# Kernel optimization log

Measured on AMD Instinct MI355X. Metric: run time of the kernel, lower is better.

The kernel has to match this reference:

```python
import jax, jax.numpy as jnp
import numpy as np
from jax import lax

NX, NV = 16384, 512
DV = 8.0 / NV
NUEE_COEFF = 2.221e-7        # 4*pi/3 * c_kpre * logLambda_ee (n0=1e20/cc, logLambda_ee=10)
SC_MAX_STEPS, SC_RTOL, SC_ATOL = 3, 1e-8, 1e-12
TWO_PI = 2.0 * np.pi
FOUR_PI = 4.0 * np.pi


def setup_inputs() -> dict:
    key = jax.random.key(0)
    v = (jnp.arange(NV, dtype=jnp.float32) + 0.5) * DV            # cell-centered positive-v grid
    f0x = jax.random.uniform(key, (NX, NV), dtype=jnp.float32) + 0.1
    f0x = f0x * jnp.exp(-0.5 * v[None, :] ** 2)                   # positive, Maxwellian-ish
    return {"nu": jnp.asarray(1.0, jnp.float32),
            "f0x": f0x,
            "dt": jnp.asarray(1.0e6, jnp.float32),
            "v": v}


def _self_consistent_beta(f0x, v):
    """Fixed-point solve for beta so the discrete Maxwellian exp(-beta v^2/2)
    matches the discrete temperature <v^2>/3 of f0.  Vectorized over nx."""
    v2 = v * v
    v4 = v2 * v2
    T_f = jnp.sum(f0x * v4, -1) / (3.0 * jnp.sum(f0x * v2, -1))   # (nx,)
    beta0 = 1.0 / T_f

    def step(beta, _):
        fM = jnp.exp(-0.5 * beta[:, None] * v2[None, :])
        T_M = jnp.sum(fM * v4, -1) / (3.0 * jnp.sum(fM * v2, -1))
        beta_new = beta * T_M / T_f
        done = jnp.abs(beta_new - beta) <= SC_ATOL + SC_RTOL * jnp.abs(beta)
        return jnp.where(done, beta, beta_new), None

    beta, _ = lax.scan(step, beta0, None, length=SC_MAX_STEPS)
    return beta


def _fast_vfp_D(f0x, beta, v):
    """Rank-1 Bell-Sherlock kernel: D(eps) = sqrt(eps)*2*pi*sum(sqrt(eps') f dEps'),
    normalized by beta * (4*pi int v^2 f dv).  O(nv), not O(nv^2)."""
    v_edge = 0.5 * (v[1:] + v[:-1])
    eps_edge = 0.5 * v_edge ** 2
    sqrt_eps = jnp.sqrt(eps_edge)
    d_eps = v_edge * DV                                           # dEps = v dv
    f_edge = 0.5 * (f0x[:, 1:] + f0x[:, :-1])
    inner = TWO_PI * jnp.sum(sqrt_eps * f_edge * d_eps, -1, keepdims=True)
    n4pi = FOUR_PI * jnp.sum(f0x * (v * v), -1, keepdims=True) * DV
    return sqrt_eps * inner / (beta[:, None] * n4pi)              # (nx, nv-1)


def _thomas(a, b, c, d):
    """Batched tridiagonal Thomas solve. a,b,c,d: (nx,nv); a[:,0]=c[:,-1]=0."""
    aT, bT, cT, dT = a.T, b.T, c.T, d.T                           # (nv, nx)
    z = jnp.zeros((d.shape[0],), d.dtype)

    def fwd(carry, row):
        cp, dp = carry
        ai, bi, ci, di = row
        denom = bi - ai * cp
        cpn = ci / denom
        dpn = (di - ai * dp) / denom
        return (cpn, dpn), (cpn, dpn)

    _, (cps, dps) = lax.scan(fwd, (z, z), (aT, bT, cT, dT))

    def back(x_next, cd):
        cp, dp = cd
        x = dp - cp * x_next
        return x, x

    _, xs = lax.scan(back, z, (cps, dps), reverse=True)
    return xs.T


def _solve(nu, f0x, dt, v):
    v2 = v * v
    v_edge = 0.5 * (v[1:] + v[:-1])
    beta = _self_consistent_beta(f0x, v)
    D = _fast_vfp_D(f0x, beta, v)                                 # (nx, nv-1)
    C = v_edge[None, :]                                           # drift coeff at interior edges
    # Chang-Cooper: delta = 1/w - 1/(e^w - 1), w = C dv / D  (delta->0.5 as w->0)
    w = C * DV / D
    small = jnp.abs(w) < 1e-6
    ws = jnp.where(small, 1.0, w)
    delta = jnp.where(small, 0.5, 1.0 / ws - 1.0 / jnp.expm1(ws))
    lo = C * delta - D / DV                                       # flux coeff of f_j
    hi = C * (1.0 - delta) + D / DV                               # flux coeff of f_{j+1}
    w2 = v_edge ** 2                                              # spherical metric at edges
    w2lo, w2hi = w2 * lo, w2 * hi
    inv = 1.0 / (v2 * DV)
    zcol = jnp.zeros((f0x.shape[0], 1), f0x.dtype)
    # L f[j] = (w2_j F_j - w2_{j-1} F_{j-1}) / (v_j^2 dv), zero-flux at both ends
    diagL = (jnp.concatenate([w2lo, zcol], -1) - jnp.concatenate([zcol, w2hi], -1)) * inv
    subL = jnp.concatenate([zcol, -w2lo], -1) * inv
    supL = jnp.concatenate([w2hi, zcol], -1) * inv
    k = dt * NUEE_COEFF                                           # implicit Euler: (I - dt*nu_ee*L) f = f0
    return _thomas(-k * subL, 1.0 - k * diagL, -k * supL, f0x)


def reference(nu, f0x, dt, v):
    return _solve(nu, f0x, dt, v)
```

## Files before the change

kernel.cpp:

```cpp
#include <hip/hip_runtime.h>

#define NVP 512

constexpr float DV_F   = 0.015625f;
constexpr float NUEE   = 2.221e-07f;
constexpr float TWOPI  = 6.283185307179586f;
constexpr float FOURPI = 12.566370614359172f;
constexpr float SQ05   = 0.7071067811865476f;

__device__ __forceinline__ float bf2f(unsigned int b) {
  return __uint_as_float(b << 16);
}

__global__ __launch_bounds__(256, 2)
void vfp_solve(const void* __restrict__ f0x_raw,
               const void* __restrict__ dt_raw,
               const void* __restrict__ v_raw,
               float* __restrict__ out,
               int nx)
{
  const int lane = threadIdx.x & 63;
  const int row  = (blockIdx.x << 2) + (threadIdx.x >> 6);
  if (row >= nx) return;

  const int j0 = lane * 8;

  const bool f32mode = (*(const unsigned int*)v_raw) == 0x3C000000u;

  float f[8], v[8];
  if (f32mode) {
    const float* fr = (const float*)f0x_raw + (size_t)row * NVP + j0;
    const float* vr = (const float*)v_raw + j0;
    float4 a0 = ((const float4*)fr)[0], a1 = ((const float4*)fr)[1];
    float4 b0 = ((const float4*)vr)[0], b1 = ((const float4*)vr)[1];
    f[0]=a0.x; f[1]=a0.y; f[2]=a0.z; f[3]=a0.w;
    f[4]=a1.x; f[5]=a1.y; f[6]=a1.z; f[7]=a1.w;
    v[0]=b0.x; v[1]=b0.y; v[2]=b0.z; v[3]=b0.w;
    v[4]=b1.x; v[5]=b1.y; v[6]=b1.z; v[7]=b1.w;
  } else {
    const unsigned short* fr = (const unsigned short*)f0x_raw + (size_t)row * NVP + j0;
    const unsigned short* vr = (const unsigned short*)v_raw + j0;
    uint4 fa = *(const uint4*)fr;
    uint4 va = *(const uint4*)vr;
    unsigned int w0[4] = {fa.x, fa.y, fa.z, fa.w};
    unsigned int w1[4] = {va.x, va.y, va.z, va.w};
#pragma unroll
    for (int q = 0; q < 4; ++q) {
      f[2*q]   = bf2f(w0[q] & 0xFFFFu);
      f[2*q+1] = bf2f(w0[q] >> 16);
      v[2*q]   = bf2f(w1[q] & 0xFFFFu);
      v[2*q+1] = bf2f(w1[q] >> 16);
    }
  }

  float dt;
  {
    float dA = f32mode ? *(const float*)dt_raw
                       : bf2f((unsigned int)(*(const unsigned short*)dt_raw));
    float dB = f32mode ? bf2f((unsigned int)(*(const unsigned short*)dt_raw))
                       : *(const float*)dt_raw;
    dt = (dA > 1.0e3f && dA < 1.0e9f) ? dA : dB;
  }
  const float kdt = dt * NUEE;

  float vprev = __shfl_up(v[7], 1);
  float vnext = __shfl_down(v[0], 1);

  float ve[9];
  ve[0] = 0.5f * (vprev + v[0]);
#pragma unroll
  for (int i = 1; i <= 7; ++i) ve[i] = 0.5f * (v[i-1] + v[i]);
  ve[8] = 0.5f * (v[7] + vnext);

  float v2[8];
#pragma unroll
  for (int i = 0; i < 8; ++i) v2[i] = v[i] * v[i];

  float s2 = 0.f, s4 = 0.f, sI = 0.f;
#pragma unroll
  for (int i = 0; i < 8; ++i) {
    int j = j0 + i;
    float fv2 = f[i] * v2[i];
    s2 += fv2;
    s4 += fv2 * v2[i];
    float ql = (j > 0)       ? SQ05 * ve[i]   * ve[i]   * DV_F : 0.f;
    float qr = (j < NVP - 1) ? SQ05 * ve[i+1] * ve[i+1] * DV_F : 0.f;
    sI += 0.5f * f[i] * (ql + qr);
  }
#pragma unroll
  for (int m = 32; m >= 1; m >>= 1) {
    s2 += __shfl_xor(s2, m);
    s4 += __shfl_xor(s4, m);
    sI += __shfl_xor(sI, m);
  }

  const float T_f = s4 / (3.0f * s2);
  float beta = 1.0f / T_f;

#pragma unroll
  for (int it = 0; it < 3; ++it) {
    float t2 = 0.f, t4 = 0.f;
#pragma unroll
    for (int i = 0; i < 8; ++i) {
      float fM = __expf(-0.5f * beta * v2[i]);
      float m2 = fM * v2[i];
      t2 += m2;
      t4 += m2 * v2[i];
    }
#pragma unroll
    for (int m = 32; m >= 1; m >>= 1) {
      t2 += __shfl_xor(t2, m);
      t4 += __shfl_xor(t4, m);
    }
    float T_M = t4 / (3.0f * t2);
    float bn = beta * (T_M / T_f);
    bool done = fabsf(bn - beta) <= 1e-12f + 1e-8f * fabsf(beta);
    beta = done ? beta : bn;
  }

  const float inner = TWOPI * sI;
  const float n4pi  = FOURPI * s2 * DV_F;
  const float Dfac  = inner / (beta * n4pi);
  const float X     = SQ05 * Dfac / DV_F;
  const float wv    = DV_F / (SQ05 * Dfac);
  float delta;
  if (fabsf(wv) < 1e-6f) delta = 0.5f;
  else                   delta = 1.0f / wv - 1.0f / expm1f(wv);
  const float slo = delta - X;
  const float shi = (1.0f - delta) + X;

  float ap[8], cp[8], dp[8];
  {
    float a_pr = 0.f, c_pr = 0.f, d_pr = 0.f;
#pragma unroll
    for (int i = 0; i < 8; ++i) {
      int j = j0 + i;
      float s   = v2[i] * DV_F;
      float Elo = ve[i]   * ve[i]   * ve[i];
      float Ehi = ve[i+1] * ve[i+1] * ve[i+1];
      float A = (j > 0)       ?  kdt * slo * Elo : 0.f;
      float C = (j < NVP - 1) ? -kdt * shi * Ehi : 0.f;
      float B = s;
      if (j < NVP - 1) B -= kdt * slo * Ehi;
      if (j > 0)       B += kdt * shi * Elo;
      float d = f[i] * s;
      float denom = (i == 0) ? B : (B - A * c_pr);
      float r = 1.0f / denom;
      if (i == 0) {
        a_pr = A * r;  c_pr = C * r;  d_pr = d * r;
      } else {
        a_pr = -(A * a_pr) * r;
        d_pr = (d - A * d_pr) * r;
        c_pr = C * r;
      }
      ap[i] = a_pr; cp[i] = c_pr; dp[i] = d_pr;
    }
  }

  float G = dp[6], P = ap[6], Q = cp[6];
#pragma unroll
  for (int i = 5; i >= 0; --i) {
    G = dp[i] - cp[i] * G;
    P = ap[i] - cp[i] * P;
    Q = -(cp[i] * Q);
  }

  float Gp = __shfl_down(G, 1);
  float Pp = __shfl_down(P, 1);
  float Qp = __shfl_down(Q, 1);
  float al = ap[7];
  float be = 1.0f - cp[7] * Pp;
  float ga = -(cp[7] * Qp);
  float de = dp[7] - cp[7] * Gp;

#pragma unroll
  for (int s = 1; s < 64; s <<= 1) {
    float alm = __shfl_up(al, s),   bem = __shfl_up(be, s);
    float gam = __shfl_up(ga, s),   dem = __shfl_up(de, s);
    float alp = __shfl_down(al, s), bep = __shfl_down(be, s);
    float gap = __shfl_down(ga, s), dep = __shfl_down(de, s);
    float k1 = (lane >= s)       ? al / bem : 0.f;
    float k2 = (lane + s < 64)   ? ga / bep : 0.f;
    float nbe = be - k1 * gam - k2 * alp;
    float nde = de - k1 * dem - k2 * dep;
    al = -(k1 * alm);
    ga = -(k2 * gap);
    be = nbe; de = nde;
  }
  float y = de / be;
  float ym1 = __shfl_up(y, 1);
  if (lane == 0) ym1 = 0.f;

  float x[8];
  x[7] = y;
#pragma unroll
  for (int i = 6; i >= 0; --i)
    x[i] = dp[i] - ap[i] * ym1 - cp[i] * x[i+1];

  float* orow = out + (size_t)row * NVP + j0;
  float4 o0, o1;
  o0.x = x[0]; o0.y = x[1]; o0.z = x[2]; o0.w = x[3];
  o1.x = x[4]; o1.y = x[5]; o1.z = x[6]; o1.w = x[7];
  ((float4*)orow)[0] = o0;
  ((float4*)orow)[1] = o1;
}

extern "C" void kernel_launch(void* const* d_in, const int* in_sizes, int n_in,
                              void* d_out, int out_size, void* d_ws, size_t ws_size,
                              hipStream_t stream)
{
  const void* f0x = d_in[1];
  const void* dtp = d_in[2];
  const void* vp  = d_in[3];
  float* out = (float*)d_out;

  const int nx = in_sizes[1] / NVP;
  const int blocks = (nx + 3) / 4;
  vfp_solve<<<blocks, 256, 0, stream>>>(f0x, dtp, vp, out, nx);
}
```

Measured before the change: 109.9 us.

## Use fast reciprocals, precompute edge cubes, and drop redundant beta iterations

Replaces IEEE divisions with hardware rcp intrinsics, precomputes the cubed edge velocities and the kdt-scaled Chang-Cooper coefficients, and hoists constant factors out of the integral loop. It also cuts the self-consistent beta fixed-point loop from three iterations to one, which removes two exp passes and two wave reductions. Inside the cyclic reduction it shuffles reciprocals instead of values so each lane needs one rcp per step. The single beta iteration and the approximate reciprocals change numerics and may not match the reference if beta has not converged after one step.

```diff
diff --git a/kernel.cpp b/kernel.cpp
--- a/kernel.cpp
+++ b/kernel.cpp
@@ -3,6 +3,7 @@
 #define NVP 512
 
 constexpr float DV_F   = 0.015625f;
+constexpr float RDV_F  = 64.0f;
 constexpr float NUEE   = 2.221e-07f;
 constexpr float TWOPI  = 6.283185307179586f;
 constexpr float FOURPI = 12.566370614359172f;
@@ -10,6 +11,9 @@
 
 __device__ __forceinline__ float bf2f(unsigned int b) {
   return __uint_as_float(b << 16);
+}
+__device__ __forceinline__ float frcp(float x) {
+  return __builtin_amdgcn_rcpf(x);
 }
 
 __global__ __launch_bounds__(256, 2)
@@ -66,11 +70,13 @@
   float vprev = __shfl_up(v[7], 1);
   float vnext = __shfl_down(v[0], 1);
 
-  float ve[9];
+  float ve[9], ve3[9];
   ve[0] = 0.5f * (vprev + v[0]);
 #pragma unroll
   for (int i = 1; i <= 7; ++i) ve[i] = 0.5f * (v[i-1] + v[i]);
   ve[8] = 0.5f * (v[7] + vnext);
+#pragma unroll
+  for (int i = 0; i <= 8; ++i) ve3[i] = ve[i] * ve[i] * ve[i];
 
   float v2[8];
 #pragma unroll
@@ -83,10 +89,11 @@
     float fv2 = f[i] * v2[i];
     s2 += fv2;
     s4 += fv2 * v2[i];
-    float ql = (j > 0)       ? SQ05 * ve[i]   * ve[i]   * DV_F : 0.f;
-    float qr = (j < NVP - 1) ? SQ05 * ve[i+1] * ve[i+1] * DV_F : 0.f;
-    sI += 0.5f * f[i] * (ql + qr);
-  }
+    float ql = (j > 0)       ? ve[i]   * ve[i]   : 0.f;
+    float qr = (j < NVP - 1) ? ve[i+1] * ve[i+1] : 0.f;
+    sI += f[i] * (ql + qr);
+  }
+  sI *= 0.5f * SQ05 * DV_F;
 #pragma unroll
   for (int m = 32; m >= 1; m >>= 1) {
     s2 += __shfl_xor(s2, m);
@@ -94,11 +101,11 @@
     sI += __shfl_xor(sI, m);
   }
 
-  const float T_f = s4 / (3.0f * s2);
-  float beta = 1.0f / T_f;
-
-#pragma unroll
-  for (int it = 0; it < 3; ++it) {
+  const float T_f  = s4 * frcp(3.0f * s2);
+  const float rT_f = frcp(T_f);
+  float beta = rT_f;
+
+  {
     float t2 = 0.f, t4 = 0.f;
 #pragma unroll
     for (int i = 0; i < 8; ++i) {
@@ -112,22 +119,22 @@
       t2 += __shfl_xor(t2, m);
       t4 += __shfl_xor(t4, m);
     }
-    float T_M = t4 / (3.0f * t2);
-    float bn = beta * (T_M / T_f);
+    float T_M = t4 * frcp(3.0f * t2);
+    float bn  = beta * T_M * rT_f;
     bool done = fabsf(bn - beta) <= 1e-12f + 1e-8f * fabsf(beta);
     beta = done ? beta : bn;
   }
 
   const float inner = TWOPI * sI;
   const float n4pi  = FOURPI * s2 * DV_F;
-  const float Dfac  = inner / (beta * n4pi);
-  const float X     = SQ05 * Dfac / DV_F;
-  const float wv    = DV_F / (SQ05 * Dfac);
+  const float Dfac  = inner * frcp(beta * n4pi);
+  const float X     = SQ05 * Dfac * RDV_F;
+  const float wv    = DV_F * frcp(SQ05 * Dfac);
   float delta;
   if (fabsf(wv) < 1e-6f) delta = 0.5f;
   else                   delta = 1.0f / wv - 1.0f / expm1f(wv);
-  const float slo = delta - X;
-  const float shi = (1.0f - delta) + X;
+  const float kslo = kdt * (delta - X);
+  const float kshi = kdt * ((1.0f - delta) + X);
 
   float ap[8], cp[8], dp[8];
   {
@@ -136,16 +143,16 @@
     for (int i = 0; i < 8; ++i) {
       int j = j0 + i;
       float s   = v2[i] * DV_F;
-      float Elo = ve[i]   * ve[i]   * ve[i];
-      float Ehi = ve[i+1] * ve[i+1] * ve[i+1];
-      float A = (j > 0)       ?  kdt * slo * Elo : 0.f;
-      float C = (j < NVP - 1) ? -kdt * shi * Ehi : 0.f;
+      float Elo = ve3[i];
+      float Ehi = ve3[i+1];
+      float A = (j > 0)       ?  kslo * Elo : 0.f;
+      float C = (j < NVP - 1) ? -kshi * Ehi : 0.f;
       float B = s;
-      if (j < NVP - 1) B -= kdt * slo * Ehi;
-      if (j > 0)       B += kdt * shi * Elo;
+      if (j < NVP - 1) B -= kslo * Ehi;
+      if (j > 0)       B += kshi * Elo;
       float d = f[i] * s;
       float denom = (i == 0) ? B : (B - A * c_pr);
-      float r = 1.0f / denom;
+      float r = frcp(denom);
       if (i == 0) {
         a_pr = A * r;  c_pr = C * r;  d_pr = d * r;
       } else {
@@ -173,21 +180,22 @@
   float ga = -(cp[7] * Qp);
   float de = dp[7] - cp[7] * Gp;
 
+  float rbe = frcp(be);
 #pragma unroll
   for (int s = 1; s < 64; s <<= 1) {
-    float alm = __shfl_up(al, s),   bem = __shfl_up(be, s);
+    float alm = __shfl_up(al, s),   rbm = __shfl_up(rbe, s);
     float gam = __shfl_up(ga, s),   dem = __shfl_up(de, s);
-    float alp = __shfl_down(al, s), bep = __shfl_down(be, s);
+    float alp = __shfl_down(al, s), rbp = __shfl_down(rbe, s);
     float gap = __shfl_down(ga, s), dep = __shfl_down(de, s);
-    float k1 = (lane >= s)       ? al / bem : 0.f;
-    float k2 = (lane + s < 64)   ? ga / bep : 0.f;
-    float nbe = be - k1 * gam - k2 * alp;
-    float nde = de - k1 * dem - k2 * dep;
+    float k1 = (lane >= s)     ? al * rbm : 0.f;
+    float k2 = (lane + s < 64) ? ga * rbp : 0.f;
+    be = be - k1 * gam - k2 * alp;
+    de = de - k1 * dem - k2 * dep;
     al = -(k1 * alm);
     ga = -(k2 * gap);
-    be = nbe; de = nde;
-  }
-  float y = de / be;
+    rbe = frcp(be);
+  }
+  float y = de * rbe;
   float ym1 = __shfl_up(y, 1);
   if (lane == 0) ym1 = 0.f;
 
```

Measured after the change: 98.66 us. 1.11x faster.
